# Performance work log

Hardware: AMD Instinct MI355X
Metric: run time of the kernel (lower is better)

## Reference

```python
import jax, jax.numpy as jnp
import numpy as np

KEEP_RATIO = 0.05


def setup_inputs() -> dict:
    key = jax.random.key(0)
    x = jax.random.normal(key, (4096, 20000), dtype=jnp.float32)
    return {"expanded_features": x}


def reference(expanded_features) -> jnp.ndarray:
    B, D = expanded_features.shape
    k = max(1, int(D * KEEP_RATIO))  # 1000
    # per-row top-k values + indices
    topk_values, topk_indices = jax.lax.top_k(expanded_features, k)  # [B, k]
    # scatter top-k values into a zero tensor (winner-take-all)
    rows = jnp.arange(B)[:, None]  # [B, 1] broadcast against [B, k]
    sparse_features = jnp.zeros_like(expanded_features).at[rows, topk_indices].set(topk_values)
    return sparse_features
```

## Files before the change

kernel.cpp:

```cpp
#include <hip/hip_runtime.h>
#include <cstdint>
#include <cstddef>

#define D_DIM 20000
#define C4    5000
#define K_SEL 1000
#define BLK   512
#define JPT   10

__device__ __forceinline__ uint32_t f2k(float f) {
    uint32_t b = __float_as_uint(f);
    return (b & 0x80000000u) ? ~b : (b | 0x80000000u);
}
__device__ __forceinline__ float k2f(uint32_t k) {
    uint32_t b = (k & 0x80000000u) ? (k & 0x7FFFFFFFu) : ~k;
    return __uint_as_float(b);
}

__global__ void __launch_bounds__(BLK)
wta_kernel(const float* __restrict__ in, float* __restrict__ out) {
    const int row  = blockIdx.x;
    const int tid  = threadIdx.x;
    const int lane = tid & 63;
    const int wid  = tid >> 6;

    __shared__ uint32_t hist[256];
    __shared__ uint32_t suf[256];
    __shared__ uint32_t bc[3];
    __shared__ uint32_t waveTot[8];

    const float4* in4  = (const float4*)(in  + (size_t)row * D_DIM);
    float4*       out4 = (float4*)      (out + (size_t)row * D_DIM);

    uint32_t keys[JPT * 4];
    #pragma unroll
    for (int j = 0; j < JPT; ++j) {
        int c = j * BLK + tid;
        if (c < C4) {
            float4 v = in4[c];
            keys[4*j+0] = f2k(v.x);
            keys[4*j+1] = f2k(v.y);
            keys[4*j+2] = f2k(v.z);
            keys[4*j+3] = f2k(v.w);
        } else {
            keys[4*j+0] = 0u; keys[4*j+1] = 0u;
            keys[4*j+2] = 0u; keys[4*j+3] = 0u;
        }
    }

    if (tid == 0) { bc[0] = 0u; bc[1] = K_SEL; bc[2] = 0u; }

    for (int p = 0; p < 4; ++p) {
        const int shift = 24 - 8 * p;
        if (tid < 256) hist[tid] = 0u;
        __syncthreads();

        const uint32_t prefix = bc[0];
        const uint32_t kp     = bc[1];
        const uint32_t maskHi = (p == 0) ? 0u : (0xFFFFFFFFu << (shift + 8));

        #pragma unroll
        for (int e = 0; e < JPT * 4; ++e) {
            uint32_t key = keys[e];
            if ((key & maskHi) == prefix)
                atomicAdd(&hist[(key >> shift) & 0xFFu], 1u);
        }
        __syncthreads();

        if (tid < 64) {
            uint32_t h0 = hist[lane*4+0], h1 = hist[lane*4+1];
            uint32_t h2 = hist[lane*4+2], h3 = hist[lane*4+3];
            uint32_t t3 = h3, t2 = h2 + t3, t1 = h1 + t2, t0 = h0 + t1;
            uint32_t tot = t0;
            uint32_t inc = tot;
            #pragma unroll
            for (int d = 1; d < 64; d <<= 1) {
                uint32_t v = __shfl_down(inc, d, 64);
                if (lane + d < 64) inc += v;
            }
            uint32_t addR = inc - tot;
            suf[lane*4+0] = t0 + addR;
            suf[lane*4+1] = t1 + addR;
            suf[lane*4+2] = t2 + addR;
            suf[lane*4+3] = t3 + addR;
        }
        __syncthreads();

        if (tid < 256) {
            uint32_t s     = suf[tid];
            uint32_t snext = (tid < 255) ? suf[tid + 1] : 0u;
            if (s >= kp && snext < kp) {
                bc[0] = prefix | ((uint32_t)tid << shift);
                bc[1] = kp - snext;
                bc[2] = s - snext;
            }
        }
        __syncthreads();
    }

    const uint32_t T      = bc[0];
    const uint32_t budget = bc[1];
    const uint32_t m      = bc[2];

    if (m == budget) {
        #pragma unroll
        for (int j = 0; j < JPT; ++j) {
            int c = j * BLK + tid;
            if (c < C4) {
                uint32_t k0 = keys[4*j+0], k1 = keys[4*j+1];
                uint32_t k2 = keys[4*j+2], k3 = keys[4*j+3];
                float4 o;
                o.x = (k0 >= T) ? k2f(k0) : 0.0f;
                o.y = (k1 >= T) ? k2f(k1) : 0.0f;
                o.z = (k2 >= T) ? k2f(k2) : 0.0f;
                o.w = (k3 >= T) ? k2f(k3) : 0.0f;
                out4[c] = o;
            }
        }
    } else {
        uint32_t running = 0;
        #pragma unroll
        for (int j = 0; j < JPT; ++j) {
            int c = j * BLK + tid;
            bool valid = (c < C4);
            uint32_t k0 = keys[4*j+0], k1 = keys[4*j+1];
            uint32_t k2 = keys[4*j+2], k3 = keys[4*j+3];
            uint32_t f0 = (valid && k0 == T) ? 1u : 0u;
            uint32_t f1 = (valid && k1 == T) ? 1u : 0u;
            uint32_t f2 = (valid && k2 == T) ? 1u : 0u;
            uint32_t f3 = (valid && k3 == T) ? 1u : 0u;
            uint32_t cnt = f0 + f1 + f2 + f3;

            uint32_t inc = cnt;
            #pragma unroll
            for (int d = 1; d < 64; d <<= 1) {
                uint32_t v = __shfl_up(inc, d, 64);
                if (lane >= d) inc += v;
            }
            if (lane == 63) waveTot[wid] = inc;
            __syncthreads();
            uint32_t waveBefore = 0, blockTot = 0;
            #pragma unroll
            for (int w = 0; w < 8; ++w) {
                uint32_t t = waveTot[w];
                blockTot += t;
                if (w < wid) waveBefore += t;
            }
            uint32_t base = running + waveBefore + (inc - cnt);
            uint32_t r0 = base;
            uint32_t r1 = base + f0;
            uint32_t r2 = base + f0 + f1;
            uint32_t r3 = base + f0 + f1 + f2;
            if (valid) {
                float4 o;
                o.x = (k0 > T || (f0 && r0 < budget)) ? k2f(k0) : 0.0f;
                o.y = (k1 > T || (f1 && r1 < budget)) ? k2f(k1) : 0.0f;
                o.z = (k2 > T || (f2 && r2 < budget)) ? k2f(k2) : 0.0f;
                o.w = (k3 > T || (f3 && r3 < budget)) ? k2f(k3) : 0.0f;
                out4[c] = o;
            }
            running += blockTot;
            __syncthreads();
        }
    }
}

extern "C" void kernel_launch(void* const* d_in, const int* in_sizes, int n_in,
                              void* d_out, int out_size, void* d_ws, size_t ws_size,
                              hipStream_t stream) {
    const float* in  = (const float*)d_in[0];
    float*       out = (float*)d_out;
    const int B = in_sizes[0] / D_DIM;
    wta_kernel<<<dim3(B), dim3(BLK), 0, stream>>>(in, out);
}
```

Baseline: 591.0 us.

## Replicate radix histograms, shrink block, and finish selection via candidate ranking

Replaces the 4-pass radix select with two 16-way-replicated histogram passes, then gathers the remaining candidates sharing the 16-bit prefix into shared memory and finds the exact threshold by brute-force ranking in one wave. It falls back to the two remaining radix passes if the candidate count exceeds 1024. The block shrinks to 256 threads with 80 keys per thread, and the output uses nontemporal stores. It aims to cut shared-memory atomic contention and synchronisation rounds, at the cost of higher register pressure, a serial O(c^2) ranking step on one wave, and a larger shared footprint.

```diff
diff --git a/kernel.cpp b/kernel.cpp
--- a/kernel.cpp
+++ b/kernel.cpp
@@ -5,8 +5,14 @@
 #define D_DIM 20000
 #define C4    5000
 #define K_SEL 1000
-#define BLK   512
-#define JPT   10
+#define BLK   256
+#define JPT   20
+#define NW    (BLK / 64)
+#define NCOPY 16
+#define CAP   1024
+
+typedef float  vf4 __attribute__((ext_vector_type(4)));
+typedef unsigned int vu4 __attribute__((ext_vector_type(4)));
 
 __device__ __forceinline__ uint32_t f2k(float f) {
     uint32_t b = __float_as_uint(f);
@@ -15,6 +21,61 @@
 __device__ __forceinline__ float k2f(uint32_t k) {
     uint32_t b = (k & 0x80000000u) ? (k & 0x7FFFFFFFu) : ~k;
     return __uint_as_float(b);
+}
+
+__device__ __forceinline__ void radix_pass(
+        const uint32_t* keys, int shift, uint32_t maskHi,
+        uint32_t* hist, volatile uint32_t* bc, uint32_t* ccnt,
+        int tid, int lane, bool zero_ccnt) {
+    uint4 z; z.x = 0u; z.y = 0u; z.z = 0u; z.w = 0u;
+    #pragma unroll
+    for (int i = 0; i < 4; ++i) ((uint4*)hist)[tid * 4 + i] = z;
+    if (zero_ccnt && tid == 0) *ccnt = 0u;
+    __syncthreads();
+
+    const uint32_t prefix = bc[0];
+    const uint32_t kp     = bc[1];
+    const int      copy   = tid & (NCOPY - 1);
+
+    #pragma unroll
+    for (int e = 0; e < JPT * 4; ++e) {
+        uint32_t key = keys[e];
+        if ((key & maskHi) == prefix)
+            atomicAdd(&hist[(((key >> shift) & 0xFFu) * NCOPY) + copy], 1u);
+    }
+    __syncthreads();
+
+    if (tid < 64) {
+        uint32_t h[4];
+        #pragma unroll
+        for (int b = 0; b < 4; ++b) {
+            const uint4* p4 = (const uint4*)&hist[(4 * lane + b) * NCOPY];
+            uint4 a = p4[0], q = p4[1], r = p4[2], s = p4[3];
+            h[b] = a.x + a.y + a.z + a.w + q.x + q.y + q.z + q.w
+                 + r.x + r.y + r.z + r.w + s.x + s.y + s.z + s.w;
+        }
+        uint32_t t3 = h[3], t2 = h[2] + t3, t1 = h[1] + t2, t0 = h[0] + t1;
+        uint32_t tot = t0;
+        uint32_t inc = tot;
+        #pragma unroll
+        for (int d = 1; d < 64; d <<= 1) {
+            uint32_t v = __shfl_down(inc, d, 64);
+            if (lane + d < 64) inc += v;
+        }
+        uint32_t addR = inc - tot;
+        uint32_t s0 = t0 + addR, s1 = t1 + addR, s2 = t2 + addR, s3 = t3 + addR;
+        uint32_t sv[4]  = { s0, s1, s2, s3 };
+        uint32_t snv[4] = { s1, s2, s3, addR };
+        #pragma unroll
+        for (int i = 0; i < 4; ++i) {
+            if (sv[i] >= kp && snv[i] < kp) {
+                bc[0] = prefix | ((uint32_t)(4 * lane + i) << shift);
+                bc[1] = kp - snv[i];
+                bc[2] = sv[i] - snv[i];
+            }
+        }
+    }
+    __syncthreads();
 }
 
 __global__ void __launch_bounds__(BLK)
@@ -24,13 +85,14 @@
     const int lane = tid & 63;
     const int wid  = tid >> 6;
 
-    __shared__ uint32_t hist[256];
-    __shared__ uint32_t suf[256];
+    __shared__ uint32_t hist[256 * NCOPY];
+    __shared__ uint32_t cand[CAP];
+    __shared__ uint32_t ccnt;
     __shared__ uint32_t bc[3];
-    __shared__ uint32_t waveTot[8];
+    __shared__ uint32_t waveTot[NW];
 
     const float4* in4  = (const float4*)(in  + (size_t)row * D_DIM);
-    float4*       out4 = (float4*)      (out + (size_t)row * D_DIM);
+    vf4*          out4 = (vf4*)         (out + (size_t)row * D_DIM);
 
     uint32_t keys[JPT * 4];
     #pragma unroll
@@ -50,52 +112,44 @@
 
     if (tid == 0) { bc[0] = 0u; bc[1] = K_SEL; bc[2] = 0u; }
 
-    for (int p = 0; p < 4; ++p) {
-        const int shift = 24 - 8 * p;
-        if (tid < 256) hist[tid] = 0u;
-        __syncthreads();
-
-        const uint32_t prefix = bc[0];
-        const uint32_t kp     = bc[1];
-        const uint32_t maskHi = (p == 0) ? 0u : (0xFFFFFFFFu << (shift + 8));
-
+    radix_pass(keys, 24, 0x00000000u, hist, bc, &ccnt, tid, lane, false);
+    radix_pass(keys, 16, 0xFF000000u, hist, bc, &ccnt, tid, lane, true);
+
+    const uint32_t prefix16 = bc[0];
+    const uint32_t kp16     = bc[1];
+    const uint32_t m16      = bc[2];
+
+    if (m16 <= CAP) {
         #pragma unroll
         for (int e = 0; e < JPT * 4; ++e) {
             uint32_t key = keys[e];
-            if ((key & maskHi) == prefix)
-                atomicAdd(&hist[(key >> shift) & 0xFFu], 1u);
+            if ((key & 0xFFFF0000u) == prefix16) {
+                uint32_t idx = atomicAdd(&ccnt, 1u);
+                if (idx < CAP) cand[idx] = key;
+            }
         }
         __syncthreads();
-
-        if (tid < 64) {
-            uint32_t h0 = hist[lane*4+0], h1 = hist[lane*4+1];
-            uint32_t h2 = hist[lane*4+2], h3 = hist[lane*4+3];
-            uint32_t t3 = h3, t2 = h2 + t3, t1 = h1 + t2, t0 = h0 + t1;
-            uint32_t tot = t0;
-            uint32_t inc = tot;
-            #pragma unroll
-            for (int d = 1; d < 64; d <<= 1) {
-                uint32_t v = __shfl_down(inc, d, 64);
-                if (lane + d < 64) inc += v;
-            }
-            uint32_t addR = inc - tot;
-            suf[lane*4+0] = t0 + addR;
-            suf[lane*4+1] = t1 + addR;
-            suf[lane*4+2] = t2 + addR;
-            suf[lane*4+3] = t3 + addR;
+        if (wid == 0) {
+            uint32_t c = ccnt;
+            for (uint32_t idx = lane; idx < c; idx += 64) {
+                uint32_t x = cand[idx];
+                uint32_t gt = 0, eq = 0;
+                for (uint32_t j = 0; j < c; ++j) {
+                    uint32_t y = cand[j];
+                    gt += (y > x) ? 1u : 0u;
+                    eq += (y == x) ? 1u : 0u;
+                }
+                if (gt < kp16 && kp16 <= gt + eq) {
+                    bc[0] = x;
+                    bc[1] = kp16 - gt;
+                    bc[2] = eq;
+                }
+            }
         }
         __syncthreads();
-
-        if (tid < 256) {
-            uint32_t s     = suf[tid];
-            uint32_t snext = (tid < 255) ? suf[tid + 1] : 0u;
-            if (s >= kp && snext < kp) {
-                bc[0] = prefix | ((uint32_t)tid << shift);
-                bc[1] = kp - snext;
-                bc[2] = s - snext;
-            }
-        }
-        __syncthreads();
+    } else {
+        radix_pass(keys, 8, 0xFFFF0000u, hist, bc, &ccnt, tid, lane, false);
+        radix_pass(keys, 0, 0xFFFFFF00u, hist, bc, &ccnt, tid, lane, false);
     }
 
     const uint32_t T      = bc[0];
@@ -109,12 +163,12 @@
             if (c < C4) {
                 uint32_t k0 = keys[4*j+0], k1 = keys[4*j+1];
                 uint32_t k2 = keys[4*j+2], k3 = keys[4*j+3];
-                float4 o;
+                vf4 o;
                 o.x = (k0 >= T) ? k2f(k0) : 0.0f;
                 o.y = (k1 >= T) ? k2f(k1) : 0.0f;
                 o.z = (k2 >= T) ? k2f(k2) : 0.0f;
                 o.w = (k3 >= T) ? k2f(k3) : 0.0f;
-                out4[c] = o;
+                __builtin_nontemporal_store(o, &out4[c]);
             }
         }
     } else {
@@ -141,7 +195,7 @@
             __syncthreads();
             uint32_t waveBefore = 0, blockTot = 0;
             #pragma unroll
-            for (int w = 0; w < 8; ++w) {
+            for (int w = 0; w < NW; ++w) {
                 uint32_t t = waveTot[w];
                 blockTot += t;
                 if (w < wid) waveBefore += t;
@@ -157,7 +211,7 @@
                 o.y = (k1 > T || (f1 && r1 < budget)) ? k2f(k1) : 0.0f;
                 o.z = (k2 > T || (f2 && r2 < budget)) ? k2f(k2) : 0.0f;
                 o.w = (k3 > T || (f3 && r3 < budget)) ? k2f(k3) : 0.0f;
-                out4[c] = o;
+                ((float4*)out4)[c] = o;
             }
             running += blockTot;
             __syncthreads();
```

Measured after the change: 558.5 us. -5.5%, faster.
